# Kernel tuning notes

Hardware: AMD Instinct MI355X
Metric: run time of the kernel (lower is better)

The kernel has to match this reference:

```python
import jax, jax.numpy as jnp
import numpy as np

B, S, H = 128, 1000, 256


def setup_inputs() -> dict:
    key = jax.random.key(0)
    ks = jax.random.split(key, 15)
    sc = 1.0 / np.sqrt(H)
    f = lambda k, shape: (jax.random.normal(k, shape, jnp.float32) * sc)
    return dict(
        static_hidden=jax.random.normal(ks[0], (B, S, H), jnp.float32),
        state_embedding=jax.random.normal(ks[1], (B, 1, H), jnp.float32),
        decoder_hidden=jax.random.normal(ks[2], (B, 1, H), jnp.float32),
        target_hidden=jax.random.normal(ks[3], (B, 1, H), jnp.float32),
        last_hh=jax.random.normal(ks[4], (1, B, H), jnp.float32),
        W_ih=f(ks[5], (3 * H, H)),
        W_hh=f(ks[6], (3 * H, H)),
        b_ih=f(ks[7], (3 * H,)),
        b_hh=f(ks[8], (3 * H,)),
        v_attn_enc=f(ks[9], (H,)),
        W_attn_enc=f(ks[10], (H, 2 * H)),
        v_attn_tgt=f(ks[11], (H,)),
        W_attn_tgt=f(ks[12], (H, 2 * H)),
        v_ptr=f(ks[13], (H,)),
        W_ptr=f(ks[14], (H, 3 * H)),
    )


def _attention(static, dec, v, W):
    # static: [B,S,H], dec: [B,1,H] -> softmax attention over S
    hid = jnp.concatenate([static, jnp.broadcast_to(dec, static.shape)], axis=2)  # [B,S,2H]
    t = jnp.tanh(jnp.einsum('hk,bsk->bhs', W, hid))  # [B,H,S]
    return jax.nn.softmax(jnp.einsum('h,bhs->bs', v, t), axis=1)  # [B,S]


def _gru_step(x, h, Wih, Whh, bih, bhh):
    # single-layer single-step torch GRU semantics; x,h: [B,H]
    gi = x @ Wih.T + bih
    gh = h @ Whh.T + bhh
    ir, iz, ig = jnp.split(gi, 3, axis=-1)
    hr, hz, hg = jnp.split(gh, 3, axis=-1)
    r = jax.nn.sigmoid(ir + hr)
    z = jax.nn.sigmoid(iz + hz)
    n = jnp.tanh(ig + r * hg)
    return (1.0 - z) * n + z * h


def _pointer_branch(static, state_emb, attn, v, W):
    context = jnp.einsum('bs,bsh->bh', attn, static)[:, None, :]  # [B,1,H]
    energy = jnp.concatenate(
        [static,
         jnp.broadcast_to(context, static.shape),
         jnp.broadcast_to(state_emb, static.shape)], axis=2)  # [B,S,3H]
    return jnp.einsum('h,bhs->bs', v, jnp.tanh(jnp.einsum('hk,bsk->bhs', W, energy)))


def reference(static_hidden, state_embedding, decoder_hidden, target_hidden, last_hh,
              W_ih, W_hh, b_ih, b_hh,
              v_attn_enc, W_attn_enc, v_attn_tgt, W_attn_tgt, v_ptr, W_ptr):
    # GRU step (dropout is identity in eval / p=0.0)
    h_new = _gru_step(decoder_hidden[:, 0, :], last_hh[0], W_ih, W_hh, b_ih, b_hh)
    rnn_out = h_new[:, None, :]  # [B,1,H]
    last_hh_new = h_new[None]    # [1,B,H]

    enc_attn = _attention(static_hidden, rnn_out, v_attn_enc, W_attn_enc)
    probs = _pointer_branch(static_hidden, state_embedding, enc_attn, v_ptr, W_ptr)

    tgt_attn = _attention(static_hidden, target_hidden, v_attn_tgt, W_attn_tgt)
    # NOTE: original code reuses self.v / self.W (not v_target/W_taret) for the
    # target branch energy -- replicated faithfully.
    probs_target = _pointer_branch(static_hidden, state_embedding, tgt_attn, v_ptr, W_ptr)

    return (5.0 * probs + probs_target, last_hh_new)
```

## Files before the change

kernel.cpp:

```cpp
#include <hip/hip_runtime.h>
#include <hip/hip_bf16.h>
#include <stdint.h>
#include <stddef.h>

#define Bn 128
#define Sn 1000
#define SP 1024
#define Hn 256

typedef __bf16 bf16;
typedef __bf16 bf16x8 __attribute__((ext_vector_type(8)));
typedef __bf16 bf16x4 __attribute__((ext_vector_type(4)));
typedef float  f32x4  __attribute__((ext_vector_type(4)));

typedef __attribute__((address_space(1))) const unsigned int* gas1;
typedef __attribute__((address_space(3))) unsigned int* las3;

__device__ __forceinline__ float fast_tanh(float x){
  return 1.0f - 2.0f / (__expf(2.0f * x) + 1.0f);
}
__device__ __forceinline__ float fast_sigmoid(float x){
  return 1.0f / (1.0f + __expf(-x));
}

__global__ void k0w(const float* __restrict__ We, const float* __restrict__ Wt,
                    const float* __restrict__ Wp, bf16* __restrict__ Wcb,
                    const float* __restrict__ dec, const float* __restrict__ lhh,
                    const float* __restrict__ tgt, const float* __restrict__ se,
                    float* __restrict__ xT, float* __restrict__ hT,
                    float* __restrict__ tT, float* __restrict__ sT){
  int blk = blockIdx.x, t = threadIdx.x;
  if (blk < 768){
    int tt = blk*256 + t;
    int r = tt >> 8, c = tt & 255;
    float val;
    if (r < 256)       val = We[r*512 + c];
    else if (r < 512)  val = Wt[(r-256)*512 + c];
    else               val = Wp[(r-512)*768 + c];
    Wcb[tt] = (bf16)val;
  } else {
    int idx = blk - 768;
    int a = idx >> 7, bb = idx & 127;
    const float* src = (a==0) ? dec : (a==1) ? lhh : (a==2) ? tgt : se;
    float* dst       = (a==0) ? xT  : (a==1) ? hT  : (a==2) ? tT  : sT;
    dst[t*128 + bb] = src[bb*256 + t];
  }
}

__global__ __launch_bounds__(512) void k1a_gru(
    const float* __restrict__ xT, const float* __restrict__ hT,
    const float* __restrict__ Wih, const float* __restrict__ Whh,
    const float* __restrict__ bih, const float* __restrict__ bhh,
    float* __restrict__ out_hh, float* __restrict__ hnT){
  int t = threadIdx.x;
  int g = t >> 7, b = t & 127;
  int h = blockIdx.x*4 + g;
  const float4* wir = (const float4*)(Wih + (size_t)h*256);
  const float4* wiz = (const float4*)(Wih + (size_t)(256+h)*256);
  const float4* wig = (const float4*)(Wih + (size_t)(512+h)*256);
  const float4* whr = (const float4*)(Whh + (size_t)h*256);
  const float4* whz = (const float4*)(Whh + (size_t)(256+h)*256);
  const float4* whg = (const float4*)(Whh + (size_t)(512+h)*256);
  float air=0.f, aiz=0.f, aig=0.f, ahr=0.f, ahz=0.f, ahg=0.f;
  #pragma unroll 2
  for (int kq=0; kq<64; kq++){
    float4 vir = wir[kq], viz = wiz[kq], vig = wig[kq];
    float4 vhr = whr[kq], vhz = whz[kq], vhg = whg[kq];
    #pragma unroll
    for (int e=0;e<4;e++){
      int k = kq*4 + e;
      float xv = xT[k*128 + b];
      float hv = hT[k*128 + b];
      float wi_r = (&vir.x)[e], wi_z = (&viz.x)[e], wi_g = (&vig.x)[e];
      float wh_r = (&vhr.x)[e], wh_z = (&vhz.x)[e], wh_g = (&vhg.x)[e];
      air += wi_r*xv; aiz += wi_z*xv; aig += wi_g*xv;
      ahr += wh_r*hv; ahz += wh_z*hv; ahg += wh_g*hv;
    }
  }
  air += bih[h];      ahr += bhh[h];
  aiz += bih[256+h];  ahz += bhh[256+h];
  aig += bih[512+h];  ahg += bhh[512+h];
  float r = fast_sigmoid(air + ahr);
  float z = fast_sigmoid(aiz + ahz);
  float n = fast_tanh(aig + r*ahg);
  float hprev = hT[h*128 + b];
  float hnew = (1.f - z)*n + z*hprev;
  out_hh[b*256 + h] = hnew;
  hnT[h*128 + b] = hnew;
}

__global__ __launch_bounds__(512) void k1c_dots(
    const float* __restrict__ hnT, const float* __restrict__ tT,
    const float* __restrict__ sT,
    const float* __restrict__ We, const float* __restrict__ Wt,
    const float* __restrict__ Wp,
    float* __restrict__ dEnc, float* __restrict__ dTgt, float* __restrict__ c3){
  int t = threadIdx.x;
  int g = t >> 7, b = t & 127;
  int vr = blockIdx.x*4 + g;
  int var = vr >> 8, h = vr & 255;
  const float* wrow; const float* X; float* dst;
  if (var == 0)      { wrow = We + (size_t)h*512 + 256; X = hnT; dst = dEnc; }
  else if (var == 1) { wrow = Wt + (size_t)h*512 + 256; X = tT;  dst = dTgt; }
  else               { wrow = Wp + (size_t)h*768 + 512; X = sT;  dst = c3; }
  const float4* w4 = (const float4*)wrow;
  float acc = 0.f;
  #pragma unroll 2
  for (int kq=0; kq<64; kq++){
    float4 wv = w4[kq];
    #pragma unroll
    for (int e=0;e<4;e++)
      acc += (&wv.x)[e] * X[(kq*4+e)*128 + b];
  }
  dst[b*256 + h] = acc;
}

__global__ __launch_bounds__(256) void k2_gemm(
    const float* __restrict__ stat, const bf16* __restrict__ Wcb,
    const float* __restrict__ dEnc, const float* __restrict__ dTgt,
    const float* __restrict__ vEnc, const float* __restrict__ vTgt,
    float* __restrict__ scE, float* __restrict__ scT, bf16* __restrict__ Aptr){
  __shared__ __align__(16) bf16 As[64*256];
  __shared__ __align__(16) bf16 Bs[256*64];
  __shared__ float pS[2][64];
  int tid = threadIdx.x, w = tid>>6, l = tid&63;
  int st = blockIdx.x, b = blockIdx.y;
  int lm = l&15, q = l>>4;
  if (tid < 128) pS[tid>>6][tid&63] = 0.f;

  {
    #pragma unroll
    for (int is=0; is<16; is++){
      int fidx = is*256 + tid;
      int row = fidx >> 6;
      int col4 = fidx & 63;
      int s = st*64 + row;
      float4 f = make_float4(0.f,0.f,0.f,0.f);
      if (s < Sn)
        f = ((const float4*)(stat + ((size_t)(b*Sn + s))*Hn))[col4];
      bf16x4 v;
      v[0]=(bf16)f.x; v[1]=(bf16)f.y; v[2]=(bf16)f.z; v[3]=(bf16)f.w;
      int c8 = col4 >> 1, half = col4 & 1;
      *(bf16x4*)(&As[row*256 + ((c8 ^ (row&7))<<3) + half*4]) = v;
    }
  }

  for (int p=0; p<3; p++){
    f32x4 acc[4][4];
    #pragma unroll
    for (int i=0;i<4;i++)
      #pragma unroll
      for (int j=0;j<4;j++) acc[i][j] = (f32x4){0.f,0.f,0.f,0.f};

    for (int kt=0; kt<4; kt++){
      __syncthreads();
      #pragma unroll
      for (int is=0; is<8; is++){
        int row = w*64 + is*8 + (l>>3);
        int sc_ = (l&7) ^ (row & 7);
        __builtin_amdgcn_global_load_lds(
            (gas1)(Wcb + ((size_t)(p*256 + row))*256 + kt*64 + sc_*8),
            (las3)(&Bs[(w*64 + is*8)*64]), 16, 0, 0);
      }
      __syncthreads();
      #pragma unroll
      for (int kk=0; kk<2; kk++){
        bf16x8 af[4], bfr[4];
        #pragma unroll
        for (int i=0;i<4;i++){
          int rA = i*16 + lm;
          int c = (kt*8 + kk*4 + q) ^ (rA & 7);
          af[i] = *(const bf16x8*)(&As[rA*256 + c*8]);
        }
        #pragma unroll
        for (int j=0;j<4;j++){
          int rB = w*64 + j*16 + lm;
          int cB = (kk*4 + q) ^ (rB & 7);
          bfr[j] = *(const bf16x8*)(&Bs[rB*64 + cB*8]);
        }
        #pragma unroll
        for (int i=0;i<4;i++)
          #pragma unroll
          for (int j=0;j<4;j++)
            acc[i][j] = __builtin_amdgcn_mfma_f32_16x16x32_bf16(af[i], bfr[j], acc[i][j], 0,0,0);
      }
    }

    if (p < 2){
      const float* vv = p ? vTgt : vEnc;
      const float* db = (p ? dTgt : dEnc) + b*256;
      float vj[4], dj[4];
      #pragma unroll
      for (int j=0;j<4;j++){
        int hh = w*64 + j*16 + lm;
        vj[j] = vv[hh]; dj[j] = db[hh];
      }
      #pragma unroll
      for (int i=0;i<4;i++){
        #pragma unroll
        for (int r=0;r<4;r++){
          float pp = 0.f;
          #pragma unroll
          for (int j=0;j<4;j++) pp += vj[j]*fast_tanh(acc[i][j][r] + dj[j]);
          pp += __shfl_xor(pp,1); pp += __shfl_xor(pp,2);
          pp += __shfl_xor(pp,4); pp += __shfl_xor(pp,8);
          if (lm == 0) atomicAdd(&pS[p][i*16 + q*4 + r], pp);
        }
      }
    } else {
      bf16* dst = Aptr + ((size_t)(b*16 + st))*16384;
      #pragma unroll
      for (int i=0;i<4;i++){
        #pragma unroll
        for (int r=0;r<4;r++){
          bf16x4 v4;
          #pragma unroll
          for (int j=0;j<4;j++) v4[j] = (bf16)acc[i][j][r];
          int slot = i*4 + r;
          *(bf16x4*)(dst + ((size_t)((slot*4 + w)*64 + l))*4) = v4;
        }
      }
    }
  }
  __syncthreads();
  if (tid < 64)        scE[b*SP + st*64 + tid]      = pS[0][tid];
  else if (tid < 128)  scT[b*SP + st*64 + tid-64]   = pS[1][tid-64];
}

__global__ __launch_bounds__(1024) void k3_ctx(
    const float* __restrict__ scE, const float* __restrict__ scT,
    const float* __restrict__ stat, float* __restrict__ ctxP){
  __shared__ float attE[500], attT[500];
  __shared__ float redE[16], redT[16];
  __shared__ float pe[4][256], pt[4][256];
  int b = blockIdx.x, sq = blockIdx.y, t = threadIdx.x;
  int wid = t>>6, ln = t&63;

  float vE = (t < Sn) ? scE[b*SP + t] : -1e30f;
  float vT = (t < Sn) ? scT[b*SP + t] : -1e30f;
  float mE = vE, mT = vT;
  #pragma unroll
  for (int o=1;o<64;o<<=1){ mE=fmaxf(mE,__shfl_xor(mE,o)); mT=fmaxf(mT,__shfl_xor(mT,o)); }
  if (ln==0){ redE[wid]=mE; redT[wid]=mT; }
  __syncthreads();
  float ME=-1e30f, MT=-1e30f;
  #pragma unroll
  for (int i=0;i<16;i++){ ME=fmaxf(ME,redE[i]); MT=fmaxf(MT,redT[i]); }
  __syncthreads();
  float eE = (t < Sn) ? __expf(vE-ME) : 0.f;
  float eT = (t < Sn) ? __expf(vT-MT) : 0.f;
  float sE=eE, sT=eT;
  #pragma unroll
  for (int o=1;o<64;o<<=1){ sE+=__shfl_xor(sE,o); sT+=__shfl_xor(sT,o); }
  if (ln==0){ redE[wid]=sE; redT[wid]=sT; }
  __syncthreads();
  float SE=0.f, ST=0.f;
  #pragma unroll
  for (int i=0;i<16;i++){ SE+=redE[i]; ST+=redT[i]; }
  float invE = 1.f/SE, invT = 1.f/ST;
  if (t < 500){
    int s = sq*500 + t;
    attE[t] = __expf(scE[b*SP+s]-ME)*invE;
    attT[t] = __expf(scT[b*SP+s]-MT)*invT;
  }
  __syncthreads();

  int sg = t>>8, h = t&255;
  const float* base = stat + ((size_t)(b*Sn + sq*500 + sg*125))*Hn + h;
  float aE=0.f, aT=0.f;
  #pragma unroll 4
  for (int i=0;i<125;i++){
    float a = base[(size_t)i*Hn];
    aE += attE[sg*125+i]*a;
    aT += attT[sg*125+i]*a;
  }
  pe[sg][h]=aE; pt[sg][h]=aT;
  __syncthreads();
  if (t < 256){
    float s0 = pe[0][t]+pe[1][t]+pe[2][t]+pe[3][t];
    ctxP[(((size_t)sq)*256 + t)*128 + b] = s0;
  } else if (t < 512){
    int h2 = t-256;
    float s1 = pt[0][h2]+pt[1][h2]+pt[2][h2]+pt[3][h2];
    ctxP[(((size_t)(2+sq))*256 + h2)*128 + b] = s1;
  }
}

__global__ __launch_bounds__(512) void k3c_c2(
    const float* __restrict__ ctxP, const float* __restrict__ Wp,
    const float* __restrict__ c3,
    float* __restrict__ cE, float* __restrict__ cT){
  int t = threadIdx.x;
  int g = t >> 7, b = t & 127;
  int vr = blockIdx.x*4 + g;
  int var = vr >> 8, h = vr & 255;
  const float4* w4 = (const float4*)(Wp + (size_t)h*768 + 256);
  const float* x0 = ctxP + ((size_t)(var*2))*256*128;
  const float* x1 = ctxP + ((size_t)(var*2+1))*256*128;
  float acc = 0.f;
  #pragma unroll 2
  for (int kq=0; kq<64; kq++){
    float4 wv = w4[kq];
    #pragma unroll
    for (int e=0;e<4;e++){
      int k = kq*4+e;
      acc += (&wv.x)[e] * (x0[k*128+b] + x1[k*128+b]);
    }
  }
  (var ? cT : cE)[b*256 + h] = acc + c3[b*256 + h];
}

__global__ __launch_bounds__(256) void k4_final(
    const bf16* __restrict__ Aptr, const float* __restrict__ cE,
    const float* __restrict__ cT, const float* __restrict__ vp,
    float* __restrict__ out){
  __shared__ float pE[64], pT[64];
  int tid=threadIdx.x, w=tid>>6, l=tid&63;
  int st=blockIdx.x, b=blockIdx.y;
  int lm=l&15, q=l>>4;
  if (tid < 64){ pE[tid]=0.f; pT[tid]=0.f; }
  __syncthreads();
  const bf16* src = Aptr + ((size_t)(b*16 + st))*16384;
  float vj[4], ej[4], tj[4];
  #pragma unroll
  for (int j=0;j<4;j++){
    int hh = w*64 + j*16 + lm;
    vj[j]=vp[hh]; ej[j]=cE[b*256+hh]; tj[j]=cT[b*256+hh];
  }
  #pragma unroll
  for (int i=0;i<4;i++){
    #pragma unroll
    for (int r=0;r<4;r++){
      int slot = i*4 + r;
      bf16x4 v4 = *(const bf16x4*)(src + ((size_t)((slot*4 + w)*64 + l))*4);
      float pe=0.f, pt=0.f;
      #pragma unroll
      for (int j=0;j<4;j++){
        float a = (float)v4[j];
        pe += vj[j]*fast_tanh(a + ej[j]);
        pt += vj[j]*fast_tanh(a + tj[j]);
      }
      pe += __shfl_xor(pe,1); pt += __shfl_xor(pt,1);
      pe += __shfl_xor(pe,2); pt += __shfl_xor(pt,2);
      pe += __shfl_xor(pe,4); pt += __shfl_xor(pt,4);
      pe += __shfl_xor(pe,8); pt += __shfl_xor(pt,8);
      if (lm==0){
        atomicAdd(&pE[i*16 + q*4 + r], pe);
        atomicAdd(&pT[i*16 + q*4 + r], pt);
      }
    }
  }
  __syncthreads();
  if (tid < 64){
    int s = st*64 + tid;
    if (s < Sn) out[b*Sn + s] = 5.0f*pE[tid] + pT[tid];
  }
}

extern "C" void kernel_launch(void* const* d_in, const int* in_sizes, int n_in,
                              void* d_out, int out_size, void* d_ws, size_t ws_size,
                              hipStream_t stream){
  const float* stat = (const float*)d_in[0];
  const float* se   = (const float*)d_in[1];
  const float* dec  = (const float*)d_in[2];
  const float* tgt  = (const float*)d_in[3];
  const float* lhh  = (const float*)d_in[4];
  const float* Wih  = (const float*)d_in[5];
  const float* Whh  = (const float*)d_in[6];
  const float* bih  = (const float*)d_in[7];
  const float* bhh  = (const float*)d_in[8];
  const float* vEnc = (const float*)d_in[9];
  const float* WEnc = (const float*)d_in[10];
  const float* vTgt = (const float*)d_in[11];
  const float* WTgt = (const float*)d_in[12];
  const float* vPtr = (const float*)d_in[13];
  const float* WPtr = (const float*)d_in[14];
  float* out = (float*)d_out;

  char* wsp = (char*)d_ws;
  bf16*  Aptr = (bf16*)(wsp);
  bf16*  Wcb  = (bf16*)(wsp + 67108864);
  float* xT   = (float*)(wsp + 67502080);
  float* hT   = (float*)(wsp + 67633152);
  float* tT   = (float*)(wsp + 67764224);
  float* sT   = (float*)(wsp + 67895296);
  float* hnT  = (float*)(wsp + 68026368);
  float* scE  = (float*)(wsp + 68157440);
  float* scT  = (float*)(wsp + 68681728);
  float* dEnc = (float*)(wsp + 69206016);
  float* dTgt = (float*)(wsp + 69337088);
  float* c3   = (float*)(wsp + 69468160);
  float* cE   = (float*)(wsp + 69599232);
  float* cT   = (float*)(wsp + 69730304);
  float* ctxP = (float*)(wsp + 69861376);

  hipLaunchKernelGGL(k0w, dim3(1280), dim3(256), 0, stream,
                     WEnc, WTgt, WPtr, Wcb, dec, lhh, tgt, se, xT, hT, tT, sT);
  hipLaunchKernelGGL(k1a_gru, dim3(64), dim3(512), 0, stream,
                     xT, hT, Wih, Whh, bih, bhh, out + Bn*Sn, hnT);
  hipLaunchKernelGGL(k1c_dots, dim3(192), dim3(512), 0, stream,
                     hnT, tT, sT, WEnc, WTgt, WPtr, dEnc, dTgt, c3);
  hipLaunchKernelGGL(k2_gemm, dim3(16, 128), dim3(256), 0, stream,
                     stat, Wcb, dEnc, dTgt, vEnc, vTgt, scE, scT, Aptr);
  hipLaunchKernelGGL(k3_ctx, dim3(128, 2), dim3(1024), 0, stream,
                     scE, scT, stat, ctxP);
  hipLaunchKernelGGL(k3c_c2, dim3(128), dim3(512), 0, stream,
                     ctxP, WPtr, c3, cE, cT);
  hipLaunchKernelGGL(k4_final, dim3(16, 128), dim3(256), 0, stream,
                     Aptr, cE, cT, vPtr, out);
}
```

Baseline: 458.4 us.

## Switch GEMM to 32x32 MFMA with 8 waves, rework context reduction via atomics

The score GEMM moves from 16x16x32 to 32x32x16 bf16 MFMA with 512-thread blocks, each wave owning a 32x64 output tile. The k4 epilogue follows the new accumulator layout, and the block size is doubled there as well. The context kernel now reads float4 rows, splits them into 16 row groups and accumulates straight into a zeroed global buffer with atomics. k3c_c2 then stages the per-batch context in LDS and runs a vectorized dot product. These steps aim to cut LDS fragment traffic and raise MFMA efficiency and memory parallelism, at the cost of an extra memset, float atomics with nondeterministic summation order, and a changed register footprint.

```diff
diff --git a/kernel.cpp b/kernel.cpp
--- a/kernel.cpp
+++ b/kernel.cpp
@@ -11,7 +11,7 @@
 typedef __bf16 bf16;
 typedef __bf16 bf16x8 __attribute__((ext_vector_type(8)));
 typedef __bf16 bf16x4 __attribute__((ext_vector_type(4)));
-typedef float  f32x4  __attribute__((ext_vector_type(4)));
+typedef float  f32x16 __attribute__((ext_vector_type(16)));
 
 typedef __attribute__((address_space(1))) const unsigned int* gas1;
 typedef __attribute__((address_space(3))) unsigned int* las3;
@@ -71,10 +71,8 @@
       int k = kq*4 + e;
       float xv = xT[k*128 + b];
       float hv = hT[k*128 + b];
-      float wi_r = (&vir.x)[e], wi_z = (&viz.x)[e], wi_g = (&vig.x)[e];
-      float wh_r = (&vhr.x)[e], wh_z = (&vhz.x)[e], wh_g = (&vhg.x)[e];
-      air += wi_r*xv; aiz += wi_z*xv; aig += wi_g*xv;
-      ahr += wh_r*hv; ahz += wh_z*hv; ahg += wh_g*hv;
+      air += (&vir.x)[e]*xv; aiz += (&viz.x)[e]*xv; aig += (&vig.x)[e]*xv;
+      ahr += (&vhr.x)[e]*hv; ahz += (&vhz.x)[e]*hv; ahg += (&vhg.x)[e]*hv;
     }
   }
   air += bih[h];      ahr += bhh[h];
@@ -115,7 +113,7 @@
   dst[b*256 + h] = acc;
 }
 
-__global__ __launch_bounds__(256) void k2_gemm(
+__global__ __launch_bounds__(512) void k2_gemm(
     const float* __restrict__ stat, const bf16* __restrict__ Wcb,
     const float* __restrict__ dEnc, const float* __restrict__ dTgt,
     const float* __restrict__ vEnc, const float* __restrict__ vTgt,
@@ -125,99 +123,87 @@
   __shared__ float pS[2][64];
   int tid = threadIdx.x, w = tid>>6, l = tid&63;
   int st = blockIdx.x, b = blockIdx.y;
-  int lm = l&15, q = l>>4;
+  int wm = (w>>2)*32, wn = (w&3)*64;
+  int l31 = l & 31, lh = l >> 5;
   if (tid < 128) pS[tid>>6][tid&63] = 0.f;
 
-  {
-    #pragma unroll
-    for (int is=0; is<16; is++){
-      int fidx = is*256 + tid;
-      int row = fidx >> 6;
-      int col4 = fidx & 63;
-      int s = st*64 + row;
-      float4 f = make_float4(0.f,0.f,0.f,0.f);
-      if (s < Sn)
-        f = ((const float4*)(stat + ((size_t)(b*Sn + s))*Hn))[col4];
-      bf16x4 v;
-      v[0]=(bf16)f.x; v[1]=(bf16)f.y; v[2]=(bf16)f.z; v[3]=(bf16)f.w;
-      int c8 = col4 >> 1, half = col4 & 1;
-      *(bf16x4*)(&As[row*256 + ((c8 ^ (row&7))<<3) + half*4]) = v;
-    }
+  #pragma unroll
+  for (int is=0; is<8; is++){
+    int fidx = is*512 + tid;
+    int row = fidx >> 6, col4 = fidx & 63;
+    int s = st*64 + row;
+    float4 f = make_float4(0.f,0.f,0.f,0.f);
+    if (s < Sn) f = ((const float4*)(stat + ((size_t)(b*Sn + s))*Hn))[col4];
+    bf16x4 v;
+    v[0]=(bf16)f.x; v[1]=(bf16)f.y; v[2]=(bf16)f.z; v[3]=(bf16)f.w;
+    int c8 = col4 >> 1, half = col4 & 1;
+    *(bf16x4*)(&As[row*256 + ((c8 ^ (row&7))<<3) + half*4]) = v;
   }
 
   for (int p=0; p<3; p++){
-    f32x4 acc[4][4];
-    #pragma unroll
-    for (int i=0;i<4;i++)
-      #pragma unroll
-      for (int j=0;j<4;j++) acc[i][j] = (f32x4){0.f,0.f,0.f,0.f};
+    f32x16 acc[2];
+    #pragma unroll
+    for (int j=0;j<2;j++)
+      #pragma unroll
+      for (int r=0;r<16;r++) acc[j][r] = 0.f;
 
     for (int kt=0; kt<4; kt++){
       __syncthreads();
       #pragma unroll
-      for (int is=0; is<8; is++){
-        int row = w*64 + is*8 + (l>>3);
-        int sc_ = (l&7) ^ (row & 7);
+      for (int is=0; is<4; is++){
+        int row = is*64 + w*8 + (l>>3);
+        int gch = (l&7) ^ (row&7);
         __builtin_amdgcn_global_load_lds(
-            (gas1)(Wcb + ((size_t)(p*256 + row))*256 + kt*64 + sc_*8),
-            (las3)(&Bs[(w*64 + is*8)*64]), 16, 0, 0);
+            (gas1)(Wcb + ((size_t)(p*256 + row))*256 + kt*64 + gch*8),
+            (las3)(&Bs[(is*64 + w*8)*64]), 16, 0, 0);
       }
       __syncthreads();
       #pragma unroll
-      for (int kk=0; kk<2; kk++){
-        bf16x8 af[4], bfr[4];
+      for (int kc=0; kc<4; kc++){
+        int rA = wm + l31;
+        int ck = kt*8 + kc*2 + lh;
+        bf16x8 af = *(const bf16x8*)(&As[rA*256 + ((ck ^ (rA&7))<<3)]);
         #pragma unroll
-        for (int i=0;i<4;i++){
-          int rA = i*16 + lm;
-          int c = (kt*8 + kk*4 + q) ^ (rA & 7);
-          af[i] = *(const bf16x8*)(&As[rA*256 + c*8]);
+        for (int j=0;j<2;j++){
+          int n = wn + j*32 + l31;
+          int ckb = kc*2 + lh;
+          bf16x8 bfv = *(const bf16x8*)(&Bs[n*64 + ((ckb ^ (n&7))<<3)]);
+          acc[j] = __builtin_amdgcn_mfma_f32_32x32x16_bf16(af, bfv, acc[j], 0,0,0);
         }
-        #pragma unroll
-        for (int j=0;j<4;j++){
-          int rB = w*64 + j*16 + lm;
-          int cB = (kk*4 + q) ^ (rB & 7);
-          bfr[j] = *(const bf16x8*)(&Bs[rB*64 + cB*8]);
-        }
-        #pragma unroll
-        for (int i=0;i<4;i++)
-          #pragma unroll
-          for (int j=0;j<4;j++)
-            acc[i][j] = __builtin_amdgcn_mfma_f32_16x16x32_bf16(af[i], bfr[j], acc[i][j], 0,0,0);
       }
     }
 
     if (p < 2){
       const float* vv = p ? vTgt : vEnc;
       const float* db = (p ? dTgt : dEnc) + b*256;
-      float vj[4], dj[4];
-      #pragma unroll
-      for (int j=0;j<4;j++){
-        int hh = w*64 + j*16 + lm;
+      float vj[2], dj[2];
+      #pragma unroll
+      for (int j=0;j<2;j++){
+        int hh = wn + j*32 + l31;
         vj[j] = vv[hh]; dj[j] = db[hh];
       }
       #pragma unroll
-      for (int i=0;i<4;i++){
-        #pragma unroll
-        for (int r=0;r<4;r++){
-          float pp = 0.f;
-          #pragma unroll
-          for (int j=0;j<4;j++) pp += vj[j]*fast_tanh(acc[i][j][r] + dj[j]);
-          pp += __shfl_xor(pp,1); pp += __shfl_xor(pp,2);
-          pp += __shfl_xor(pp,4); pp += __shfl_xor(pp,8);
-          if (lm == 0) atomicAdd(&pS[p][i*16 + q*4 + r], pp);
+      for (int r=0;r<16;r++){
+        float pp = vj[0]*fast_tanh(acc[0][r] + dj[0])
+                 + vj[1]*fast_tanh(acc[1][r] + dj[1]);
+        pp += __shfl_xor(pp,1); pp += __shfl_xor(pp,2);
+        pp += __shfl_xor(pp,4); pp += __shfl_xor(pp,8); pp += __shfl_xor(pp,16);
+        if (l31 == 0){
+          int row = wm + (r&3) + 8*(r>>2) + 4*lh;
+          atomicAdd(&pS[p][row], pp);
         }
       }
     } else {
       bf16* dst = Aptr + ((size_t)(b*16 + st))*16384;
       #pragma unroll
-      for (int i=0;i<4;i++){
+      for (int j=0;j<2;j++){
         #pragma unroll
-        for (int r=0;r<4;r++){
+        for (int q4=0;q4<4;q4++){
           bf16x4 v4;
           #pragma unroll
-          for (int j=0;j<4;j++) v4[j] = (bf16)acc[i][j][r];
-          int slot = i*4 + r;
-          *(bf16x4*)(dst + ((size_t)((slot*4 + w)*64 + l))*4) = v4;
+          for (int rr=0;rr<4;rr++) v4[rr] = (bf16)acc[j][q4*4+rr];
+          int slot = w*8 + j*4 + q4;
+          *(bf16x4*)(dst + ((size_t)(slot*64 + l))*4) = v4;
         }
       }
     }
@@ -229,11 +215,11 @@
 
 __global__ __launch_bounds__(1024) void k3_ctx(
     const float* __restrict__ scE, const float* __restrict__ scT,
-    const float* __restrict__ stat, float* __restrict__ ctxP){
+    const float* __restrict__ stat, float* __restrict__ ctxG){
   __shared__ float attE[500], attT[500];
   __shared__ float redE[16], redT[16];
-  __shared__ float pe[4][256], pt[4][256];
-  int b = blockIdx.x, sq = blockIdx.y, t = threadIdx.x;
+  __shared__ float4 pe4[16][64], pt4[16][64];
+  int b = blockIdx.x, sg = blockIdx.y, t = threadIdx.x;
   int wid = t>>6, ln = t&63;
 
   float vE = (t < Sn) ? scE[b*SP + t] : -1e30f;
@@ -259,95 +245,118 @@
   for (int i=0;i<16;i++){ SE+=redE[i]; ST+=redT[i]; }
   float invE = 1.f/SE, invT = 1.f/ST;
   if (t < 500){
-    int s = sq*500 + t;
+    int s = sg*500 + t;
     attE[t] = __expf(scE[b*SP+s]-ME)*invE;
     attT[t] = __expf(scT[b*SP+s]-MT)*invT;
   }
   __syncthreads();
 
-  int sg = t>>8, h = t&255;
-  const float* base = stat + ((size_t)(b*Sn + sq*500 + sg*125))*Hn + h;
-  float aE=0.f, aT=0.f;
+  int h4 = t & 63, rg = t >> 6;
+  float4 aE = make_float4(0.f,0.f,0.f,0.f), aT = aE;
+  int nrows = (rg == 15) ? 20 : 32;
+  const float4* base = (const float4*)(stat + ((size_t)(b*Sn + sg*500 + rg*32))*Hn) + h4;
   #pragma unroll 4
-  for (int i=0;i<125;i++){
-    float a = base[(size_t)i*Hn];
-    aE += attE[sg*125+i]*a;
-    aT += attT[sg*125+i]*a;
-  }
-  pe[sg][h]=aE; pt[sg][h]=aT;
-  __syncthreads();
-  if (t < 256){
-    float s0 = pe[0][t]+pe[1][t]+pe[2][t]+pe[3][t];
-    ctxP[(((size_t)sq)*256 + t)*128 + b] = s0;
-  } else if (t < 512){
-    int h2 = t-256;
-    float s1 = pt[0][h2]+pt[1][h2]+pt[2][h2]+pt[3][h2];
-    ctxP[(((size_t)(2+sq))*256 + h2)*128 + b] = s1;
+  for (int i=0;i<nrows;i++){
+    float4 f = base[(size_t)i*64];
+    float wE = attE[rg*32 + i], wT = attT[rg*32 + i];
+    aE.x += wE*f.x; aE.y += wE*f.y; aE.z += wE*f.z; aE.w += wE*f.w;
+    aT.x += wT*f.x; aT.y += wT*f.y; aT.z += wT*f.z; aT.w += wT*f.w;
+  }
+  pe4[rg][h4] = aE; pt4[rg][h4] = aT;
+  __syncthreads();
+  if (t < 64){
+    float4 s = make_float4(0.f,0.f,0.f,0.f);
+    #pragma unroll
+    for (int i=0;i<16;i++){
+      float4 p = pe4[i][t];
+      s.x+=p.x; s.y+=p.y; s.z+=p.z; s.w+=p.w;
+    }
+    atomicAdd(&ctxG[b*256 + t*4 + 0], s.x);
+    atomicAdd(&ctxG[b*256 + t*4 + 1], s.y);
+    atomicAdd(&ctxG[b*256 + t*4 + 2], s.z);
+    atomicAdd(&ctxG[b*256 + t*4 + 3], s.w);
+  } else if (t < 128){
+    int h = t - 64;
+    float4 s = make_float4(0.f,0.f,0.f,0.f);
+    #pragma unroll
+    for (int i=0;i<16;i++){
+      float4 p = pt4[i][h];
+      s.x+=p.x; s.y+=p.y; s.z+=p.z; s.w+=p.w;
+    }
+    atomicAdd(&ctxG[32768 + b*256 + h*4 + 0], s.x);
+    atomicAdd(&ctxG[32768 + b*256 + h*4 + 1], s.y);
+    atomicAdd(&ctxG[32768 + b*256 + h*4 + 2], s.z);
+    atomicAdd(&ctxG[32768 + b*256 + h*4 + 3], s.w);
   }
 }
 
 __global__ __launch_bounds__(512) void k3c_c2(
-    const float* __restrict__ ctxP, const float* __restrict__ Wp,
+    const float* __restrict__ ctxG, const float* __restrict__ Wp,
     const float* __restrict__ c3,
     float* __restrict__ cE, float* __restrict__ cT){
-  int t = threadIdx.x;
-  int g = t >> 7, b = t & 127;
-  int vr = blockIdx.x*4 + g;
-  int var = vr >> 8, h = vr & 255;
+  __shared__ __align__(16) float ctxL[512];
+  int b = blockIdx.x, t = threadIdx.x;
+  ctxL[t] = ctxG[(t>>8)*32768 + b*256 + (t&255)];
+  __syncthreads();
+  int var = t >> 8, h = t & 255;
   const float4* w4 = (const float4*)(Wp + (size_t)h*768 + 256);
-  const float* x0 = ctxP + ((size_t)(var*2))*256*128;
-  const float* x1 = ctxP + ((size_t)(var*2+1))*256*128;
+  const float4* cv = (const float4*)(&ctxL[var*256]);
   float acc = 0.f;
-  #pragma unroll 2
-  for (int kq=0; kq<64; kq++){
-    float4 wv = w4[kq];
-    #pragma unroll
-    for (int e=0;e<4;e++){
-      int k = kq*4+e;
-      acc += (&wv.x)[e] * (x0[k*128+b] + x1[k*128+b]);
-    }
+  #pragma unroll 4
+  for (int k=0;k<64;k++){
+    float4 wv = w4[k], xv = cv[k];
+    acc += wv.x*xv.x + wv.y*xv.y + wv.z*xv.z + wv.w*xv.w;
   }
   (var ? cT : cE)[b*256 + h] = acc + c3[b*256 + h];
 }
 
-__global__ __launch_bounds__(256) void k4_final(
+__global__ __launch_bounds__(512) void k4_final(
     const bf16* __restrict__ Aptr, const float* __restrict__ cE,
     const float* __restrict__ cT, const float* __restrict__ vp,
     float* __restrict__ out){
   __shared__ float pE[64], pT[64];
   int tid=threadIdx.x, w=tid>>6, l=tid&63;
   int st=blockIdx.x, b=blockIdx.y;
-  int lm=l&15, q=l>>4;
-  if (tid < 64){ pE[tid]=0.f; pT[tid]=0.f; }
+  int wm=(w>>2)*32, wn=(w&3)*64;
+  int l31=l&31, lh=l>>5;
+  if (tid < 128){ (tid<64 ? pE : pT)[tid&63] = 0.f; }
   __syncthreads();
   const bf16* src = Aptr + ((size_t)(b*16 + st))*16384;
-  float vj[4], ej[4], tj[4];
-  #pragma unroll
-  for (int j=0;j<4;j++){
-    int hh = w*64 + j*16 + lm;
+  float vj[2], ej[2], tj[2];
+  #pragma unroll
+  for (int j=0;j<2;j++){
+    int hh = wn + j*32 + l31;
     vj[j]=vp[hh]; ej[j]=cE[b*256+hh]; tj[j]=cT[b*256+hh];
   }
-  #pragma unroll
-  for (int i=0;i<4;i++){
-    #pragma unroll
-    for (int r=0;r<4;r++){
-      int slot = i*4 + r;
-      bf16x4 v4 = *(const bf16x4*)(src + ((size_t)((slot*4 + w)*64 + l))*4);
-      float pe=0.f, pt=0.f;
-      #pragma unroll
-      for (int j=0;j<4;j++){
-        float a = (float)v4[j];
-        pe += vj[j]*fast_tanh(a + ej[j]);
-        pt += vj[j]*fast_tanh(a + tj[j]);
-      }
-      pe += __shfl_xor(pe,1); pt += __shfl_xor(pt,1);
-      pe += __shfl_xor(pe,2); pt += __shfl_xor(pt,2);
-      pe += __shfl_xor(pe,4); pt += __shfl_xor(pt,4);
-      pe += __shfl_xor(pe,8); pt += __shfl_xor(pt,8);
-      if (lm==0){
-        atomicAdd(&pE[i*16 + q*4 + r], pe);
-        atomicAdd(&pT[i*16 + q*4 + r], pt);
-      }
+  float peR[16], ptR[16];
+  #pragma unroll
+  for (int r=0;r<16;r++){ peR[r]=0.f; ptR[r]=0.f; }
+  #pragma unroll
+  for (int j=0;j<2;j++){
+    #pragma unroll
+    for (int q4=0;q4<4;q4++){
+      int slot = w*8 + j*4 + q4;
+      bf16x4 v4 = *(const bf16x4*)(src + ((size_t)(slot*64 + l))*4);
+      #pragma unroll
+      for (int rr=0;rr<4;rr++){
+        float a = (float)v4[rr];
+        peR[q4*4+rr] += vj[j]*fast_tanh(a + ej[j]);
+        ptR[q4*4+rr] += vj[j]*fast_tanh(a + tj[j]);
+      }
+    }
+  }
+  #pragma unroll
+  for (int r=0;r<16;r++){
+    float pe = peR[r], pt = ptR[r];
+    pe += __shfl_xor(pe,1); pt += __shfl_xor(pt,1);
+    pe += __shfl_xor(pe,2); pt += __shfl_xor(pt,2);
+    pe += __shfl_xor(pe,4); pt += __shfl_xor(pt,4);
+    pe += __shfl_xor(pe,8); pt += __shfl_xor(pt,8);
+    pe += __shfl_xor(pe,16); pt += __shfl_xor(pt,16);
+    if (l31 == 0){
+      int row = wm + (r&3) + 8*(r>>2) + 4*lh;
+      atomicAdd(&pE[row], pe);
+      atomicAdd(&pT[row], pt);
     }
   }
   __syncthreads();
@@ -392,20 +401,21 @@
   float* c3   = (float*)(wsp + 69468160);
   float* cE   = (float*)(wsp + 69599232);
   float* cT   = (float*)(wsp + 69730304);
-  float* ctxP = (float*)(wsp + 69861376);
-
+  float* ctxG = (float*)(wsp + 69861376);
+
+  hipMemsetAsync(ctxG, 0, 262144, stream);
   hipLaunchKernelGGL(k0w, dim3(1280), dim3(256), 0, stream,
                      WEnc, WTgt, WPtr, Wcb, dec, lhh, tgt, se, xT, hT, tT, sT);
   hipLaunchKernelGGL(k1a_gru, dim3(64), dim3(512), 0, stream,
                      xT, hT, Wih, Whh, bih, bhh, out + Bn*Sn, hnT);
   hipLaunchKernelGGL(k1c_dots, dim3(192), dim3(512), 0, stream,
                      hnT, tT, sT, WEnc, WTgt, WPtr, dEnc, dTgt, c3);
-  hipLaunchKernelGGL(k2_gemm, dim3(16, 128), dim3(256), 0, stream,
+  hipLaunchKernelGGL(k2_gemm, dim3(16, 128), dim3(512), 0, stream,
                      stat, Wcb, dEnc, dTgt, vEnc, vTgt, scE, scT, Aptr);
   hipLaunchKernelGGL(k3_ctx, dim3(128, 2), dim3(1024), 0, stream,
-                     scE, scT, stat, ctxP);
+                     scE, scT, stat, ctxG);
   hipLaunchKernelGGL(k3c_c2, dim3(128), dim3(512), 0, stream,
-                     ctxP, WPtr, c3, cE, cT);
-  hipLaunchKernelGGL(k4_final, dim3(16, 128), dim3(256), 0, stream,
+                     ctxG, WPtr, c3, cE, cT);
+  hipLaunchKernelGGL(k4_final, dim3(16, 128), dim3(512), 0, stream,
                      Aptr, cE, cT, vPtr, out);
 }
```

Measured after the change: 444.5 us. 1.03x faster.
